# Kernel tuning notes

Hardware: AMD Instinct MI355X
Metric: run time of the kernel (lower is better)

The kernel has to match this reference:

```python
import jax, jax.numpy as jnp
import numpy as np

LN_EPS = 1e-5
LOG_EPS = 1e-8

def _layernorm(x, w, b):
    mu = jnp.mean(x, axis=-1, keepdims=True)
    var = jnp.mean((x - mu) ** 2, axis=-1, keepdims=True)
    return (x - mu) * jax.lax.rsqrt(var + LN_EPS) * w + b


def setup_inputs() -> dict:
    key = jax.random.key(0)
    ks = jax.random.split(key, 8)
    B, T, D = 4, 4096, 1024
    x = jax.random.normal(ks[0], (B, T, D), dtype=jnp.float32)
    ln_w = jnp.ones((D,), jnp.float32)
    ln_b = jnp.zeros((D,), jnp.float32)
    # torch Linear stores weight as (out, in)
    Wf = jax.random.normal(ks[1], (D, D), jnp.float32) / np.sqrt(D)
    bf = jax.random.normal(ks[2], (D,), jnp.float32) * 0.02
    # module inits reach to zeros; use small random values for a non-trivial baseline
    Wr = jax.random.normal(ks[3], (D, D), jnp.float32) * 0.02
    br = jax.random.normal(ks[4], (D,), jnp.float32) * 0.02
    alpha_bias = jnp.array([3.0], jnp.float32) + jax.random.normal(ks[5], (1,), jnp.float32) * 0.1
    beta_scale = jnp.array([0.02], jnp.float32)
    return {"x": x, "ln_w": ln_w, "ln_b": ln_b, "Wf": Wf, "bf": bf,
            "Wr": Wr, "br": br, "alpha_bias": alpha_bias, "beta_scale": beta_scale}


def reference(x, ln_w, ln_b, Wf, bf, Wr, br, alpha_bias, beta_scale):
    residual = x
    x_norm = _layernorm(x, ln_w, ln_b)                       # [B,T,D]
    alpha = jax.nn.sigmoid(jnp.einsum('btd,ed->bte', x_norm, Wf) + bf + alpha_bias)
    beta_x = beta_scale * (1.0 - alpha) * x_norm
    log_alpha = jnp.log(alpha + LOG_EPS)
    log_alpha_cumsum = jnp.cumsum(log_alpha, axis=1)          # [B,T,D]
    m = jnp.max(log_alpha_cumsum, axis=1, keepdims=True)      # [B,1,D]
    scale = jnp.exp(log_alpha_cumsum - m)
    x_star = beta_x * scale
    s_star = jnp.cumsum(x_star, axis=1)
    output = s_star / (scale + LOG_EPS)
    x_gate = jnp.tanh(jnp.einsum('btd,ed->bte', output, Wr) + br)
    return x_gate * 0.05 + residual
```

## Files before the change

### kernel.cpp

```cpp
#include <hip/hip_runtime.h>

#define D_DIM 1024
#define B_DIM 4
#define T_DIM 4096
#define M_DIM (B_DIM * T_DIM)
#define CHUNK 32
#define NCHUNK (T_DIM / CHUNK)
#define NWAVE_C 16
#define SEG (NCHUNK / NWAVE_C)
#define NKT (D_DIM / 64)

typedef unsigned short u16;
typedef __attribute__((ext_vector_type(8))) __bf16 bf16x8;
typedef __attribute__((ext_vector_type(4))) float f32x4;

__device__ __forceinline__ float bf2f(u16 u) {
    union { unsigned int i; float f; } v;
    v.i = ((unsigned int)u) << 16;
    return v.f;
}
__device__ __forceinline__ u16 f2bf(float f) {
    union { float f; unsigned int i; } v;
    v.f = f;
    unsigned int u = v.i;
    unsigned int r = (u + 0x7fffu + ((u >> 16) & 1u)) >> 16;
    return (u16)r;
}
__device__ __forceinline__ float fast_tanh(float v) {
    float e = __expf(2.f * v);
    return 1.f - 2.f / (e + 1.f);
}

#define GLOAD16(g, l)                                                   \
    __builtin_amdgcn_global_load_lds(                                   \
        (const __attribute__((address_space(1))) void*)(g),             \
        (__attribute__((address_space(3))) void*)(l), 16, 0, 0)

#define BAR()                                      \
    do {                                           \
        asm volatile("" ::: "memory");             \
        __builtin_amdgcn_s_barrier();              \
        asm volatile("" ::: "memory");             \
    } while (0)

#define WAITVM(N) asm volatile("s_waitcnt vmcnt(" #N ")" ::: "memory")

__global__ __launch_bounds__(256) void ln_conv_kernel(const float* __restrict__ x,
                                                      const float* __restrict__ w,
                                                      const float* __restrict__ b,
                                                      u16* __restrict__ xn,
                                                      const float* __restrict__ Wf,
                                                      const float* __restrict__ Wr,
                                                      u16* __restrict__ da,
                                                      u16* __restrict__ db) {
    int tid = threadIdx.x;
    if (blockIdx.x < 2048) {
        int i = blockIdx.x * 256 + tid;
        const float* s = (i < 262144) ? Wf : Wr;
        u16* dp = (i < 262144) ? da : db;
        int j = i & 262143;
        float4 v = ((const float4*)s)[j];
        ushort4 o;
        o.x = f2bf(v.x); o.y = f2bf(v.y); o.z = f2bf(v.z); o.w = f2bf(v.w);
        ((ushort4*)dp)[j] = o;
        return;
    }
    int wv = tid >> 6, lane = tid & 63;
    int row = (blockIdx.x - 2048) * 4 + wv;
    const float4* xr = (const float4*)(x + (size_t)row * D_DIM);
    float4 xv[4];
    #pragma unroll
    for (int k = 0; k < 4; k++) xv[k] = xr[lane + 64 * k];
    float s = 0.f, s2 = 0.f;
    #pragma unroll
    for (int k = 0; k < 4; k++) {
        s  += xv[k].x + xv[k].y + xv[k].z + xv[k].w;
        s2 += xv[k].x * xv[k].x + xv[k].y * xv[k].y
            + xv[k].z * xv[k].z + xv[k].w * xv[k].w;
    }
    #pragma unroll
    for (int o = 1; o < 64; o <<= 1) {
        s  += __shfl_xor(s, o, 64);
        s2 += __shfl_xor(s2, o, 64);
    }
    float mu = s * (1.0f / D_DIM);
    float var = s2 * (1.0f / D_DIM) - mu * mu;
    float rs = rsqrtf(var + 1e-5f);
    ushort4* xo = (ushort4*)(xn + (size_t)row * D_DIM);
    #pragma unroll
    for (int k = 0; k < 4; k++) {
        float4 wv4 = ((const float4*)w)[lane + 64 * k];
        float4 bv4 = ((const float4*)b)[lane + 64 * k];
        ushort4 o;
        o.x = f2bf((xv[k].x - mu) * rs * wv4.x + bv4.x);
        o.y = f2bf((xv[k].y - mu) * rs * wv4.y + bv4.y);
        o.z = f2bf((xv[k].z - mu) * rs * wv4.z + bv4.z);
        o.w = f2bf((xv[k].w - mu) * rs * wv4.w + bv4.w);
        xo[lane + 64 * k] = o;
    }
}

__device__ __forceinline__ void gemm256_core(const u16* __restrict__ AG,
                                             const u16* __restrict__ BG,
                                             int tile_m, int tile_n,
                                             u16* ldsA, u16* ldsB,
                                             f32x4 (*acc)[4]) {
    int tid  = threadIdx.x;
    int wave = tid >> 6, lane = tid & 63;
    int wr = wave >> 2, wc = wave & 3;
    int q = lane >> 4;
    int srow = tid >> 3;
    int scol = ((tid & 7) ^ (srow & 7)) * 8;
    const u16* gA = AG + (size_t)(tile_m + srow) * D_DIM + scol;
    const u16* gB = BG + (size_t)(tile_n + srow) * D_DIM + scol;
    int ldst = wave * 512;
    int aRow = wr * 128 + (lane & 15);
    int bRow = wc * 64 + (lane & 15);
    int x7 = lane & 7;
    int s0 = (q ^ x7) * 8;
    int s1 = ((4 | q) ^ x7) * 8;

#define STG4(ldsbase, gsrc, koff)                                        \
    do {                                                                 \
        _Pragma("unroll") for (int j = 0; j < 4; j++)                    \
            GLOAD16((gsrc) + (size_t)j * (64 * D_DIM) + (koff),          \
                    (ldsbase) + j * 4096 + ldst);                        \
    } while (0)

#define MMQ(Af, Bf, mo, no)                                              \
    do {                                                                 \
        __builtin_amdgcn_s_setprio(1);                                   \
        _Pragma("unroll") for (int ks_ = 0; ks_ < 2; ks_++)              \
            _Pragma("unroll") for (int mi_ = 0; mi_ < 4; mi_++)          \
                _Pragma("unroll") for (int ni_ = 0; ni_ < 2; ni_++)      \
                    acc[(mo) + mi_][(no) + ni_] =                        \
                        __builtin_amdgcn_mfma_f32_16x16x32_bf16(         \
                            Af[mi_][ks_], Bf[ni_][ks_],                  \
                            acc[(mo) + mi_][(no) + ni_], 0, 0, 0);       \
        __builtin_amdgcn_s_setprio(0);                                   \
    } while (0)

    STG4(ldsA, gA, 0);
    STG4(ldsB, gB, 0);
    STG4(ldsA + 16384, gA, 64);
    STG4(ldsB + 16384, gB, 64);
    WAITVM(8);
    BAR();

    for (int t = 0; t < NKT; t++) {
        int c = t & 1;
        const u16* pA = ldsA + c * 16384 + aRow * 64;
        const u16* pB = ldsB + c * 16384 + bRow * 64;
        bf16x8 A0[4][2], A1[4][2], B0[2][2], B1[2][2];
        #pragma unroll
        for (int mi = 0; mi < 4; mi++) {
            A0[mi][0] = *(const bf16x8*)(pA + mi * 1024 + s0);
            A0[mi][1] = *(const bf16x8*)(pA + mi * 1024 + s1);
        }
        #pragma unroll
        for (int ni = 0; ni < 2; ni++) {
            B0[ni][0] = *(const bf16x8*)(pB + ni * 1024 + s0);
            B0[ni][1] = *(const bf16x8*)(pB + ni * 1024 + s1);
        }
        MMQ(A0, B0, 0, 0);
        #pragma unroll
        for (int mi = 0; mi < 4; mi++) {
            A1[mi][0] = *(const bf16x8*)(pA + (mi + 4) * 1024 + s0);
            A1[mi][1] = *(const bf16x8*)(pA + (mi + 4) * 1024 + s1);
        }
        #pragma unroll
        for (int ni = 0; ni < 2; ni++) {
            B1[ni][0] = *(const bf16x8*)(pB + (ni + 2) * 1024 + s0);
            B1[ni][1] = *(const bf16x8*)(pB + (ni + 2) * 1024 + s1);
        }
        MMQ(A0, B1, 0, 2);
        BAR();
        if (t + 2 < NKT) STG4(ldsA + c * 16384, gA, (size_t)(t + 2) * 64);
        MMQ(A1, B0, 4, 0);
        if (t + 2 < NKT) {
            STG4(ldsB + c * 16384, gB, (size_t)(t + 2) * 64);
            WAITVM(8);
        } else {
            WAITVM(0);
        }
        BAR();
        MMQ(A1, B1, 4, 2);
    }
#undef STG4
#undef MMQ
}

__global__ __launch_bounds__(512, 2) void gemm1_kernel(const u16* __restrict__ xn,
                                                       const u16* __restrict__ Wfc,
                                                       const float* __restrict__ bf_,
                                                       const float* __restrict__ ab,
                                                       const float* __restrict__ bs,
                                                       u16* __restrict__ out_la,
                                                       float* __restrict__ Sg,
                                                       float* __restrict__ Tg) {
    __shared__ __align__(16) u16 ldsA[2][16384];
    __shared__ __align__(16) u16 ldsB[2][16384];
    int flat = blockIdx.y * 4 + blockIdx.x;
    int xcd = flat & 7, p = flat >> 3;
    int tile_m = (xcd * 8 + (p >> 2)) * 256;
    int tile_n = (p & 3) * 256;
    f32x4 acc[8][4] = {};
    gemm256_core(xn, Wfc, tile_m, tile_n, &ldsA[0][0], &ldsB[0][0], acc);

    int tid = threadIdx.x, wave = tid >> 6, lane = tid & 63;
    int wr = wave >> 2, wc = wave & 3;
    float abv = ab[0], bsv = bs[0];
    int q = lane >> 4, l = lane & 15;
    #pragma unroll
    for (int ni = 0; ni < 4; ni++) {
        int col = tile_n + wc * 64 + ni * 16 + l;
        float bcol = bf_[col];
        #pragma unroll
        for (int ch = 0; ch < 4; ch++) {
            float lav[2][4], bxv[2][4];
            #pragma unroll
            for (int h = 0; h < 2; h++) {
                int mi = 2 * ch + h;
                #pragma unroll
                for (int r = 0; r < 4; r++) {
                    int row = tile_m + wr * 128 + mi * 16 + q * 4 + r;
                    float z = acc[mi][ni][r] + bcol + abv;
                    float alpha = 1.f / (1.f + __expf(-z));
                    float la_ = __logf(alpha + 1e-8f);
                    float xv = bf2f(xn[(size_t)row * D_DIM + col]);
                    lav[h][r] = la_;
                    bxv[h][r] = bsv * (1.f - alpha) * xv;
                    out_la[(size_t)row * D_DIM + col] = f2bf(la_);
                }
            }
            float s0 = lav[0][0] + lav[0][1] + lav[0][2] + lav[0][3];
            float s1 = lav[1][0] + lav[1][1] + lav[1][2] + lav[1][3];
            float x0 = s0, x1 = s1, y;
            y = __shfl_up(x0, 16, 64); if (q >= 1) x0 += y;
            y = __shfl_up(x0, 32, 64); if (q >= 2) x0 += y;
            y = __shfl_up(x1, 16, 64); if (q >= 1) x1 += y;
            y = __shfl_up(x1, 32, 64); if (q >= 2) x1 += y;
            float t0 = __shfl(x0, l + 48, 64);
            float t1 = __shfl(x1, l + 48, 64);
            float e0 = x0 - s0, e1 = x1 - s1;
            float pr = e0, Tp = 0.f;
            #pragma unroll
            for (int r = 0; r < 4; r++) { pr += lav[0][r]; Tp += bxv[0][r] * __expf(pr); }
            pr = t0 + e1;
            #pragma unroll
            for (int r = 0; r < 4; r++) { pr += lav[1][r]; Tp += bxv[1][r] * __expf(pr); }
            Tp += __shfl_xor(Tp, 16, 64);
            Tp += __shfl_xor(Tp, 32, 64);
            if (q == 0) {
                int cidx = ((tile_m + wr * 128) >> 5) + ch;
                Sg[(size_t)cidx * D_DIM + col] = t0 + t1;
                Tg[(size_t)cidx * D_DIM + col] = Tp;
            }
        }
    }
}

__global__ __launch_bounds__(1024) void scan_combine(const u16* __restrict__ la,
                                                     const float* __restrict__ S,
                                                     const float* __restrict__ Tb,
                                                     float* __restrict__ Of,
                                                     float* __restrict__ SSp) {
    __shared__ float lsS[NWAVE_C][64], lsW[NWAVE_C][64];
    int b = blockIdx.x >> 4;
    int dg = blockIdx.x & 15;
    int wave = threadIdx.x >> 6, lane = threadIdx.x & 63;
    int d = dg * 64 + lane;
    float m = bf2f(la[(size_t)(b * T_DIM) * D_DIM + d]);
    size_t base = ((size_t)b * NCHUNK) * D_DIM + d;
    int c0 = wave * SEG;

    float OfR[SEG], wR[SEG];
    float Or = 0.f, w = 0.f;
    #pragma unroll
    for (int j = 0; j < SEG; j++) {
        size_t ci = base + (size_t)(c0 + j) * D_DIM;
        OfR[j] = Or;
        wR[j]  = w;
        w  += __expf(Or) * Tb[ci];
        Or += S[ci];
    }
    lsS[wave][lane] = Or; lsW[wave][lane] = w;
    __syncthreads();

    float o = 0.f, s = 0.f, myO = 0.f, myS = 0.f;
    #pragma unroll
    for (int w2 = 0; w2 < NWAVE_C; w2++) {
        if (w2 == wave) { myO = o; myS = s; }
        s += __expf(o - m) * lsW[w2][lane];
        o += lsS[w2][lane];
    }

    float em = __expf(myO - m);
    #pragma unroll
    for (int j = 0; j < SEG; j++) {
        size_t ci = base + (size_t)(c0 + j) * D_DIM;
        Of[ci]  = myO + OfR[j] - m;
        SSp[ci] = myS + em * wR[j];
    }
}

__global__ __launch_bounds__(256) void scan_final(const u16* __restrict__ la,
                                                  const u16* __restrict__ xn,
                                                  const float* __restrict__ bs,
                                                  const float* __restrict__ Of,
                                                  const float* __restrict__ SSp,
                                                  u16* __restrict__ osc) {
    int bc = blockIdx.x;
    int b = bc >> 7, c = bc & (NCHUNK - 1);
    int col0 = threadIdx.x * 4;
    float bsv = bs[0];
    size_t base = ((size_t)(b * T_DIM + c * CHUNK)) * D_DIM + col0;
    size_t ci = ((size_t)(b * NCHUNK + c)) * D_DIM + col0;
    float ofs[4], ss[4], p[4];
    #pragma unroll
    for (int j = 0; j < 4; j++) { ofs[j] = Of[ci + j]; ss[j] = SSp[ci + j]; p[j] = 0.f; }
    #pragma unroll 8
    for (int t = 0; t < CHUNK; t++) {
        size_t idx = base + (size_t)t * D_DIM;
        ushort4 lv = *(const ushort4*)(la + idx);
        ushort4 xv = *(const ushort4*)(xn + idx);
        u16 lvs[4] = {lv.x, lv.y, lv.z, lv.w};
        u16 xvs[4] = {xv.x, xv.y, xv.z, xv.w};
        u16 os[4];
        #pragma unroll
        for (int j = 0; j < 4; j++) {
            float lav = bf2f(lvs[j]);
            p[j] += lav;
            float scv = __expf(ofs[j] + p[j]);
            float bx = bsv * (1.f - __expf(lav)) * bf2f(xvs[j]);
            ss[j] += bx * scv;
            os[j] = f2bf(ss[j] / (scv + 1e-8f));
        }
        ushort4 o; o.x = os[0]; o.y = os[1]; o.z = os[2]; o.w = os[3];
        *(ushort4*)(osc + idx) = o;
    }
}

__global__ __launch_bounds__(512, 2) void gemm2_kernel(const u16* __restrict__ A,
                                                       const u16* __restrict__ Bm,
                                                       const float* __restrict__ bias,
                                                       const float* __restrict__ resid,
                                                       float* __restrict__ out_f) {
    __shared__ __align__(16) u16 ldsA[2][16384];
    __shared__ __align__(16) u16 ldsB[2][16384];
    int flat = blockIdx.y * 4 + blockIdx.x;
    int xcd = flat & 7, p = flat >> 3;
    int tile_m = (xcd * 8 + (p >> 2)) * 256;
    int tile_n = (p & 3) * 256;
    f32x4 acc[8][4] = {};
    gemm256_core(A, Bm, tile_m, tile_n, &ldsA[0][0], &ldsB[0][0], acc);

    int tid = threadIdx.x, wave = tid >> 6, lane = tid & 63;
    int wr = wave >> 2, wc = wave & 3;
    int q = lane >> 4, l = lane & 15;
    #pragma unroll
    for (int mi = 0; mi < 8; mi++) {
        #pragma unroll
        for (int r = 0; r < 4; r++) {
            int row = tile_m + wr * 128 + mi * 16 + q * 4 + r;
            #pragma unroll
            for (int ni = 0; ni < 4; ni++) {
                int col = tile_n + wc * 64 + ni * 16 + l;
                size_t idx = (size_t)row * D_DIM + col;
                float g = fast_tanh(acc[mi][ni][r] + bias[col]);
                out_f[idx] = 0.05f * g + resid[idx];
            }
        }
    }
}

extern "C" void kernel_launch(void* const* d_in, const int* in_sizes, int n_in,
                              void* d_out, int out_size, void* d_ws, size_t ws_size,
                              hipStream_t stream) {
    const float* x   = (const float*)d_in[0];
    const float* lnw = (const float*)d_in[1];
    const float* lnb = (const float*)d_in[2];
    const float* Wf  = (const float*)d_in[3];
    const float* bf_ = (const float*)d_in[4];
    const float* Wr  = (const float*)d_in[5];
    const float* br  = (const float*)d_in[6];
    const float* ab  = (const float*)d_in[7];
    const float* bs  = (const float*)d_in[8];
    float* out = (float*)d_out;

    char* w = (char*)d_ws;
    u16* xn  = (u16*)w;
    u16* la  = (u16*)(w + (size_t)33554432);
    u16* Wfc = (u16*)(w + (size_t)67108864);
    u16* Wrc = (u16*)(w + (size_t)69206016);
    float* S   = (float*)(w + (size_t)71303168);
    float* Tb  = S  + 524288;
    float* Of  = Tb + 524288;
    float* SSp = Of + 524288;
    u16* osc = xn;

    ln_conv_kernel<<<dim3(2048 + M_DIM / 4), dim3(256), 0, stream>>>(
        x, lnw, lnb, xn, Wf, Wr, Wfc, Wrc);
    gemm1_kernel<<<dim3(D_DIM / 256, M_DIM / 256), dim3(512), 0, stream>>>(
        xn, Wfc, bf_, ab, bs, la, S, Tb);
    scan_combine<<<dim3(B_DIM * 16), dim3(1024), 0, stream>>>(la, S, Tb, Of, SSp);
    scan_final<<<dim3(B_DIM * NCHUNK), dim3(256), 0, stream>>>(la, xn, bs, Of, SSp, osc);
    gemm2_kernel<<<dim3(D_DIM / 256, M_DIM / 256), dim3(512), 0, stream>>>(
        osc, Wrc, br, x, out);
}
```

Before: 273.3 us.

## Reschedule GEMM mainloop with extra barriers and split staging around MFMA quadrants

Restructures the double-buffered GEMM main loop into a ping-pong style schedule. LDS fragment reads for both halves happen up front, barriers separate the read and compute phases, and global-to-LDS staging is split into half-tile chunks interleaved between MFMA quadrants. The aim is better overlap of memory traffic with matrix cores and better coordination between waves. The extra barriers per iteration add synchronization cost, and the reordered wait counts risk stalls or hazards.

```diff
diff --git a/kernel.cpp b/kernel.cpp
--- a/kernel.cpp
+++ b/kernel.cpp
@@ -120,11 +120,28 @@
     int s0 = (q ^ x7) * 8;
     int s1 = ((4 | q) ^ x7) * 8;
 
-#define STG4(ldsbase, gsrc, koff)                                        \
-    do {                                                                 \
-        _Pragma("unroll") for (int j = 0; j < 4; j++)                    \
-            GLOAD16((gsrc) + (size_t)j * (64 * D_DIM) + (koff),          \
-                    (ldsbase) + j * 4096 + ldst);                        \
+#define STG2(ldsb, gsrc, koff, half)                                         \
+    do {                                                                     \
+        GLOAD16((gsrc) + (size_t)((half) * 128) * D_DIM + (koff),            \
+                (ldsb) + (half) * 8192 + ldst);                              \
+        GLOAD16((gsrc) + (size_t)((half) * 128 + 64) * D_DIM + (koff),       \
+                (ldsb) + (half) * 8192 + 4096 + ldst);                       \
+    } while (0)
+
+#define RD4A(dst, base, mo)                                                  \
+    do {                                                                     \
+        _Pragma("unroll") for (int mi_ = 0; mi_ < 4; mi_++) {                \
+            dst[mi_][0] = *(const bf16x8*)((base) + ((mo) + mi_) * 1024 + s0); \
+            dst[mi_][1] = *(const bf16x8*)((base) + ((mo) + mi_) * 1024 + s1); \
+        }                                                                    \
+    } while (0)
+
+#define RD2B(dst, base, no)                                                  \
+    do {                                                                     \
+        _Pragma("unroll") for (int ni_ = 0; ni_ < 2; ni_++) {                \
+            dst[ni_][0] = *(const bf16x8*)((base) + ((no) + ni_) * 1024 + s0); \
+            dst[ni_][1] = *(const bf16x8*)((base) + ((no) + ni_) * 1024 + s1); \
+        }                                                                    \
     } while (0)
 
 #define MMQ(Af, Bf, mo, no)                                              \
@@ -140,53 +157,43 @@
         __builtin_amdgcn_s_setprio(0);                                   \
     } while (0)
 
-    STG4(ldsA, gA, 0);
-    STG4(ldsB, gB, 0);
-    STG4(ldsA + 16384, gA, 64);
-    STG4(ldsB + 16384, gB, 64);
+    STG2(ldsB, gB, 0, 0); STG2(ldsA, gA, 0, 0); STG2(ldsA, gA, 0, 1); STG2(ldsB, gB, 0, 1);
+    STG2(ldsB + 16384, gB, 64, 0); STG2(ldsA + 16384, gA, 64, 0);
+    STG2(ldsA + 16384, gA, 64, 1); STG2(ldsB + 16384, gB, 64, 1);
     WAITVM(8);
     BAR();
 
     for (int t = 0; t < NKT; t++) {
-        int c = t & 1;
-        const u16* pA = ldsA + c * 16384 + aRow * 64;
-        const u16* pB = ldsB + c * 16384 + bRow * 64;
+        const int cur = t & 1;
+        const u16* pA = ldsA + cur * 16384 + aRow * 64;
+        const u16* pB = ldsB + cur * 16384 + bRow * 64;
+        u16* dA = ldsA + cur * 16384;
+        u16* dB = ldsB + cur * 16384;
+        const bool stg = (t + 2 < NKT);
+        const size_t ko = (size_t)(t + 2) * 64;
         bf16x8 A0[4][2], A1[4][2], B0[2][2], B1[2][2];
-        #pragma unroll
-        for (int mi = 0; mi < 4; mi++) {
-            A0[mi][0] = *(const bf16x8*)(pA + mi * 1024 + s0);
-            A0[mi][1] = *(const bf16x8*)(pA + mi * 1024 + s1);
-        }
-        #pragma unroll
-        for (int ni = 0; ni < 2; ni++) {
-            B0[ni][0] = *(const bf16x8*)(pB + ni * 1024 + s0);
-            B0[ni][1] = *(const bf16x8*)(pB + ni * 1024 + s1);
-        }
+        RD4A(A0, pA, 0);
+        RD2B(B0, pB, 0);
+        BAR();
         MMQ(A0, B0, 0, 0);
-        #pragma unroll
-        for (int mi = 0; mi < 4; mi++) {
-            A1[mi][0] = *(const bf16x8*)(pA + (mi + 4) * 1024 + s0);
-            A1[mi][1] = *(const bf16x8*)(pA + (mi + 4) * 1024 + s1);
-        }
-        #pragma unroll
-        for (int ni = 0; ni < 2; ni++) {
-            B1[ni][0] = *(const bf16x8*)(pB + (ni + 2) * 1024 + s0);
-            B1[ni][1] = *(const bf16x8*)(pB + (ni + 2) * 1024 + s1);
-        }
+        BAR();
+        RD4A(A1, pA, 4);
+        RD2B(B1, pB, 2);
+        BAR();
+        MMQ(A1, B1, 4, 2);
+        BAR();
+        if (stg) { STG2(dA, gA, ko, 0); STG2(dA, gA, ko, 1); STG2(dB, gB, ko, 0); }
+        MMQ(A1, B0, 4, 0);
+        BAR();
+        if (stg) STG2(dB, gB, ko, 1);
         MMQ(A0, B1, 0, 2);
-        BAR();
-        if (t + 2 < NKT) STG4(ldsA + c * 16384, gA, (size_t)(t + 2) * 64);
-        MMQ(A1, B0, 4, 0);
-        if (t + 2 < NKT) {
-            STG4(ldsB + c * 16384, gB, (size_t)(t + 2) * 64);
-            WAITVM(8);
-        } else {
-            WAITVM(0);
-        }
-        BAR();
-        MMQ(A1, B1, 4, 2);
-    }
-#undef STG4
+        if (t + 2 < NKT) { WAITVM(8); }
+        else if (t + 1 < NKT) { WAITVM(0); }
+        BAR();
+    }
+#undef STG2
+#undef RD4A
+#undef RD2B
 #undef MMQ
 }
 
```

Result: no change. 278.3 us (+1.8%).

## Restructure GEMM mainloop to 4-stage K=32 pipeline and stage x tile via LDS

Applied to the files above, without the earlier changes.

The shared 256x256 GEMM core now uses K-steps of 32 with a 4-deep LDS ring buffer and prefetch distance 3, replacing the 2-stage K=64 split-MMQ schedule with a single batch of 32 MFMAs per step. The aim is to hide global-load latency better and simplify scheduling, at the cost of twice as many barriers per K. The gemm1 epilogue also stages its xn tile into LDS with coalesced async loads instead of scattered per-element global bf16 reads. The wait counts for the pipeline tail are rewritten, so correctness depends on the new vmcnt bookkeeping.

```diff
diff --git a/kernel.cpp b/kernel.cpp
--- a/kernel.cpp
+++ b/kernel.cpp
@@ -8,7 +8,7 @@
 #define NCHUNK (T_DIM / CHUNK)
 #define NWAVE_C 16
 #define SEG (NCHUNK / NWAVE_C)
-#define NKT (D_DIM / 64)
+#define NKT (D_DIM / 32)
 
 typedef unsigned short u16;
 typedef __attribute__((ext_vector_type(8))) __bf16 bf16x8;
@@ -108,86 +108,57 @@
     int tid  = threadIdx.x;
     int wave = tid >> 6, lane = tid & 63;
     int wr = wave >> 2, wc = wave & 3;
-    int q = lane >> 4;
-    int srow = tid >> 3;
-    int scol = ((tid & 7) ^ (srow & 7)) * 8;
-    const u16* gA = AG + (size_t)(tile_m + srow) * D_DIM + scol;
-    const u16* gB = BG + (size_t)(tile_n + srow) * D_DIM + scol;
-    int ldst = wave * 512;
-    int aRow = wr * 128 + (lane & 15);
-    int bRow = wc * 64 + (lane & 15);
-    int x7 = lane & 7;
-    int s0 = (q ^ x7) * 8;
-    int s1 = ((4 | q) ^ x7) * 8;
-
-#define STG4(ldsbase, gsrc, koff)                                        \
-    do {                                                                 \
-        _Pragma("unroll") for (int j = 0; j < 4; j++)                    \
-            GLOAD16((gsrc) + (size_t)j * (64 * D_DIM) + (koff),          \
-                    (ldsbase) + j * 4096 + ldst);                        \
+    int lrow = lane >> 2;
+    int sswz = (lane & 3) ^ (lrow & 3);
+    const u16* gA = AG + (size_t)(tile_m + wave * 32 + lrow) * D_DIM + sswz * 8;
+    const u16* gB = BG + (size_t)(tile_n + wave * 32 + lrow) * D_DIM + sswz * 8;
+    int ldst = wave * 1024 + lane * 8;
+    int fr = lane & 15, q = lane >> 4;
+    int sw = (q ^ (lane & 3)) * 8;
+    const u16* pAb = ldsA + (wr * 128 + fr) * 32 + sw;
+    const u16* pBb = ldsB + (wc * 64 + fr) * 32 + sw;
+
+#define STG(ldsb, gsrc, tt)                                                  \
+    do {                                                                     \
+        GLOAD16((gsrc) + (size_t)(tt) * 32,                                  \
+                (ldsb) + ((tt) & 3) * 8192 + ldst);                          \
+        GLOAD16((gsrc) + (size_t)(tt) * 32 + (size_t)16 * D_DIM,             \
+                (ldsb) + ((tt) & 3) * 8192 + 512 + ldst);                    \
     } while (0)
 
-#define MMQ(Af, Bf, mo, no)                                              \
-    do {                                                                 \
-        __builtin_amdgcn_s_setprio(1);                                   \
-        _Pragma("unroll") for (int ks_ = 0; ks_ < 2; ks_++)              \
-            _Pragma("unroll") for (int mi_ = 0; mi_ < 4; mi_++)          \
-                _Pragma("unroll") for (int ni_ = 0; ni_ < 2; ni_++)      \
-                    acc[(mo) + mi_][(no) + ni_] =                        \
-                        __builtin_amdgcn_mfma_f32_16x16x32_bf16(         \
-                            Af[mi_][ks_], Bf[ni_][ks_],                  \
-                            acc[(mo) + mi_][(no) + ni_], 0, 0, 0);       \
-        __builtin_amdgcn_s_setprio(0);                                   \
-    } while (0)
-
-    STG4(ldsA, gA, 0);
-    STG4(ldsB, gB, 0);
-    STG4(ldsA + 16384, gA, 64);
-    STG4(ldsB + 16384, gB, 64);
+    STG(ldsA, gA, 0); STG(ldsB, gB, 0);
+    STG(ldsA, gA, 1); STG(ldsB, gB, 1);
+    STG(ldsA, gA, 2); STG(ldsB, gB, 2);
     WAITVM(8);
     BAR();
 
     for (int t = 0; t < NKT; t++) {
-        int c = t & 1;
-        const u16* pA = ldsA + c * 16384 + aRow * 64;
-        const u16* pB = ldsB + c * 16384 + bRow * 64;
-        bf16x8 A0[4][2], A1[4][2], B0[2][2], B1[2][2];
-        #pragma unroll
-        for (int mi = 0; mi < 4; mi++) {
-            A0[mi][0] = *(const bf16x8*)(pA + mi * 1024 + s0);
-            A0[mi][1] = *(const bf16x8*)(pA + mi * 1024 + s1);
-        }
-        #pragma unroll
-        for (int ni = 0; ni < 2; ni++) {
-            B0[ni][0] = *(const bf16x8*)(pB + ni * 1024 + s0);
-            B0[ni][1] = *(const bf16x8*)(pB + ni * 1024 + s1);
-        }
-        MMQ(A0, B0, 0, 0);
-        #pragma unroll
-        for (int mi = 0; mi < 4; mi++) {
-            A1[mi][0] = *(const bf16x8*)(pA + (mi + 4) * 1024 + s0);
-            A1[mi][1] = *(const bf16x8*)(pA + (mi + 4) * 1024 + s1);
-        }
-        #pragma unroll
-        for (int ni = 0; ni < 2; ni++) {
-            B1[ni][0] = *(const bf16x8*)(pB + (ni + 2) * 1024 + s0);
-            B1[ni][1] = *(const bf16x8*)(pB + (ni + 2) * 1024 + s1);
-        }
-        MMQ(A0, B1, 0, 2);
-        BAR();
-        if (t + 2 < NKT) STG4(ldsA + c * 16384, gA, (size_t)(t + 2) * 64);
-        MMQ(A1, B0, 4, 0);
-        if (t + 2 < NKT) {
-            STG4(ldsB + c * 16384, gB, (size_t)(t + 2) * 64);
+        const int c = t & 3;
+        const u16* pA = pAb + c * 8192;
+        const u16* pB = pBb + c * 8192;
+        bf16x8 Af[8], Bf[4];
+        #pragma unroll
+        for (int ni = 0; ni < 4; ni++) Bf[ni] = *(const bf16x8*)(pB + ni * 512);
+        #pragma unroll
+        for (int mi = 0; mi < 8; mi++) Af[mi] = *(const bf16x8*)(pA + mi * 512);
+        #pragma unroll
+        for (int mi = 0; mi < 8; mi++)
+            #pragma unroll
+            for (int ni = 0; ni < 4; ni++)
+                acc[mi][ni] = __builtin_amdgcn_mfma_f32_16x16x32_bf16(
+                    Af[mi], Bf[ni], acc[mi][ni], 0, 0, 0);
+        if (t + 3 < NKT) {
+            STG(ldsA, gA, t + 3);
+            STG(ldsB, gB, t + 3);
             WAITVM(8);
-        } else {
+        } else if (t + 2 < NKT) {
+            WAITVM(4);
+        } else if (t + 1 < NKT) {
             WAITVM(0);
         }
         BAR();
-        MMQ(A1, B1, 4, 2);
-    }
-#undef STG4
-#undef MMQ
+    }
+#undef STG
 }
 
 __global__ __launch_bounds__(512, 2) void gemm1_kernel(const u16* __restrict__ xn,
@@ -198,19 +169,30 @@
                                                        u16* __restrict__ out_la,
                                                        float* __restrict__ Sg,
                                                        float* __restrict__ Tg) {
-    __shared__ __align__(16) u16 ldsA[2][16384];
-    __shared__ __align__(16) u16 ldsB[2][16384];
+    __shared__ __align__(16) u16 lds[65536];
+    u16* ldsA = lds;
+    u16* ldsB = lds + 32768;
     int flat = blockIdx.y * 4 + blockIdx.x;
     int xcd = flat & 7, p = flat >> 3;
     int tile_m = (xcd * 8 + (p >> 2)) * 256;
     int tile_n = (p & 3) * 256;
     f32x4 acc[8][4] = {};
-    gemm256_core(xn, Wfc, tile_m, tile_n, &ldsA[0][0], &ldsB[0][0], acc);
+    gemm256_core(xn, Wfc, tile_m, tile_n, ldsA, ldsB, acc);
 
     int tid = threadIdx.x, wave = tid >> 6, lane = tid & 63;
     int wr = wave >> 2, wc = wave & 3;
+    int q = lane >> 4, l = lane & 15;
+    #pragma unroll
+    for (int j = 0; j < 16; j++) {
+        int xrow = wave * 32 + j * 2 + (lane >> 5);
+        int xslot = (lane & 31) ^ (xrow & 3);
+        GLOAD16(xn + (size_t)(tile_m + xrow) * D_DIM + tile_n + xslot * 8,
+                lds + wave * 8192 + j * 512 + lane * 8);
+    }
+    WAITVM(0);
+    BAR();
+
     float abv = ab[0], bsv = bs[0];
-    int q = lane >> 4, l = lane & 15;
     #pragma unroll
     for (int ni = 0; ni < 4; ni++) {
         int col = tile_n + wc * 64 + ni * 16 + l;
@@ -223,11 +205,13 @@
                 int mi = 2 * ch + h;
                 #pragma unroll
                 for (int r = 0; r < 4; r++) {
-                    int row = tile_m + wr * 128 + mi * 16 + q * 4 + r;
+                    int rl = wr * 128 + mi * 16 + q * 4 + r;
+                    int cl = wc * 64 + ni * 16 + l;
+                    int row = tile_m + rl;
                     float z = acc[mi][ni][r] + bcol + abv;
                     float alpha = 1.f / (1.f + __expf(-z));
                     float la_ = __logf(alpha + 1e-8f);
-                    float xv = bf2f(xn[(size_t)row * D_DIM + col]);
+                    float xv = bf2f(lds[rl * 256 + (((cl >> 3) ^ (rl & 3)) * 8) + (cl & 7)]);
                     lav[h][r] = la_;
                     bxv[h][r] = bsv * (1.f - alpha) * xv;
                     out_la[(size_t)row * D_DIM + col] = f2bf(la_);
@@ -346,14 +330,15 @@
                                                        const float* __restrict__ bias,
                                                        const float* __restrict__ resid,
                                                        float* __restrict__ out_f) {
-    __shared__ __align__(16) u16 ldsA[2][16384];
-    __shared__ __align__(16) u16 ldsB[2][16384];
+    __shared__ __align__(16) u16 lds[65536];
+    u16* ldsA = lds;
+    u16* ldsB = lds + 32768;
     int flat = blockIdx.y * 4 + blockIdx.x;
     int xcd = flat & 7, p = flat >> 3;
     int tile_m = (xcd * 8 + (p >> 2)) * 256;
     int tile_n = (p & 3) * 256;
     f32x4 acc[8][4] = {};
-    gemm256_core(A, Bm, tile_m, tile_n, &ldsA[0][0], &ldsB[0][0], acc);
+    gemm256_core(A, Bm, tile_m, tile_n, ldsA, ldsB, acc);
 
     int tid = threadIdx.x, wave = tid >> 6, lane = tid & 63;
     int wr = wave >> 2, wc = wave & 3;
```

After: 268.6 us. About the same (-1.7%).
